# Performance work log

Hardware: AMD Instinct MI355X
Metric: run time of the kernel (lower is better)

The kernel has to match this reference:

```python
import jax, jax.numpy as jnp
import numpy as np

IN_F, OUT_F, LAT, RES, K, B = 512, 512, 512, 64, 3, 8
EPS = 1e-08
C_LIN = 1.0 / np.sqrt(LAT)          # EqualizedWeight scale for linear
C_CONV = 1.0 / np.sqrt(IN_F * K * K)  # EqualizedWeight scale for conv


def setup_inputs() -> dict:
    key = jax.random.key(0)
    k1, k2, k3, k4 = jax.random.split(key, 4)
    return {
        "x": jax.random.normal(k1, (B, IN_F, RES, RES), dtype=jnp.float32),
        "latent": jax.random.normal(k2, (B, LAT), dtype=jnp.float32),
        "w_lin": jax.random.normal(k3, (IN_F, LAT), dtype=jnp.float32),
        "b_lin": jnp.ones((IN_F,), dtype=jnp.float32),
        "w_conv": jax.random.normal(k4, (OUT_F, IN_F, K, K), dtype=jnp.float32),
        "b_conv": jnp.zeros((OUT_F,), dtype=jnp.float32),
    }


def reference(x, latent, w_lin, b_lin, w_conv, b_conv):
    # EqualizedLinear: s = latent @ (w_lin*c).T + b_lin*lr_mul  -> [B, IN_F]
    s = latent @ (w_lin * C_LIN).T + b_lin
    # ModulatedConv2d. Per-sample weight w[b,o,i,k,k] = (w_conv*c)[o,i,k,k]*s[b,i],
    # demodulated by sigma_inv[b,o] = rsqrt(sum_{i,k,k} w^2 + eps).
    w = w_conv * C_CONV  # [O, I, K, K]
    # sum_{k,k} w^2 over spatial -> [O, I], then contract with s^2 -> [B, O]
    w2 = jnp.sum(w * w, axis=(2, 3))  # [O, I]
    sigma_inv = jax.lax.rsqrt(jnp.einsum('oi,bi->bo', w2, s * s) + EPS)
    # conv(x, w*s_b) == conv(x * s_b, w): modulate input, single batched conv,
    # then demodulate output per (b, o). Avoids materializing B*O filters.
    x_mod = x * s[:, :, None, None]
    y = jax.lax.conv_general_dilated(
        x_mod, w,
        window_strides=(1, 1),
        padding=[((K - 1) // 2, (K - 1) // 2)] * 2,
        dimension_numbers=('NCHW', 'OIHW', 'NCHW'),
    )
    y = y * sigma_inv[:, :, None, None] + b_conv[None, :, None, None]
    return y
```

## Files before the change

### kernel.cpp

```cpp
#include <hip/hip_runtime.h>
#include <hip/hip_bf16.h>

#define IN_F 512
#define OUT_F 512
#define LATD 512
#define RES 64
#define BATCH 8
#define EPSV 1e-8f

static constexpr float C_LIN  = 0.04419417382415922f;
static constexpr float C_CONV = 0.014731391274719739f;

typedef __attribute__((ext_vector_type(8)))  short short8;
typedef __attribute__((ext_vector_type(16))) float f32x16;

union BF { __hip_bfloat16 h; short s; };

__device__ __forceinline__ void async_load16(const char* g, char* l) {
  __builtin_amdgcn_global_load_lds(
      (const __attribute__((address_space(1))) unsigned int*)g,
      (__attribute__((address_space(3))) unsigned int*)l, 16, 0, 0);
}

__global__ void k_prep(const float* __restrict__ w_conv,
                       short* __restrict__ wb,
                       float* __restrict__ w2,
                       char* __restrict__ xmp,
                       const float* __restrict__ latent,
                       const float* __restrict__ w_lin,
                       const float* __restrict__ b_lin,
                       float* __restrict__ s) {
  const int t = blockIdx.x * 256 + threadIdx.x;
  {
    const int o = t >> 9;
    const int i = t & 511;
    const float* src = w_conv + (size_t)t * 9;
    const int c = i >> 4, hf0 = (i >> 3) & 1, ch = i & 7;
    const int ob = o >> 7, ol = o & 127;
    short* dst = wb + (size_t)(c * 4 + ob) * 18432 + hf0 * 1024 + ol * 8 + ch;
    float sum = 0.f;
#pragma unroll
    for (int tap = 0; tap < 9; ++tap) {
      const float v = src[tap] * C_CONV;
      sum += v * v;
      BF cv; cv.h = __float2bfloat16(v);
      dst[tap * 2048] = cv.s;
    }
    w2[t] = sum;
  }

  if (blockIdx.x < 256) {
    char* base = xmp + (size_t)blockIdx.x * 139392;
    for (int q = threadIdx.x; q < 520; q += 256) {
      int h, hf, w;
      if (q < 132)      { h = 0;  hf = (q >= 66) ? 1 : 0; w = q - hf * 66; }
      else if (q < 264) { const int r = q - 132; h = 65; hf = (r >= 66) ? 1 : 0; w = r - hf * 66; }
      else              { const int r = q - 264; h = (r >> 2) + 1; hf = (r >> 1) & 1; w = (r & 1) * 65; }
      *(uint4*)(base + ((size_t)(h * 132 + hf * 66 + w)) * 16) = make_uint4(0u, 0u, 0u, 0u);
    }
  }

  if (blockIdx.x < 128) {
    const int wv = threadIdx.x >> 6, lane = threadIdx.x & 63;
    const int i = blockIdx.x * 4 + wv;
    const float4* wl = (const float4*)(w_lin + (size_t)i * LATD);
    const float4 w0 = wl[lane * 2], w1 = wl[lane * 2 + 1];
    float acc[BATCH];
#pragma unroll
    for (int b = 0; b < BATCH; ++b) {
      const float4* lt = (const float4*)(latent + (size_t)b * LATD);
      const float4 l0 = lt[lane * 2], l1 = lt[lane * 2 + 1];
      acc[b] = w0.x * l0.x + w0.y * l0.y + w0.z * l0.z + w0.w * l0.w +
               w1.x * l1.x + w1.y * l1.y + w1.z * l1.z + w1.w * l1.w;
    }
#pragma unroll
    for (int b = 0; b < BATCH; ++b) {
      float v = acc[b];
#pragma unroll
      for (int off = 32; off > 0; off >>= 1) v += __shfl_down(v, off);
      if (lane == 0) s[b * IN_F + i] = v * C_LIN + b_lin[i];
    }
  }
}

__global__ void k_mod_sigma(const float* __restrict__ x,
                            const float* __restrict__ s,
                            char* __restrict__ xmp,
                            const float* __restrict__ w2,
                            float* __restrict__ sigma_inv) {
  if (blockIdx.x < 128) {
    const int o = blockIdx.x * 4 + (threadIdx.x >> 6);
    const int lane = threadIdx.x & 63;
    float acc[BATCH];
#pragma unroll
    for (int b = 0; b < BATCH; ++b) acc[b] = 0.f;
#pragma unroll
    for (int k = 0; k < 8; ++k) {
      const int i = k * 64 + lane;
      const float w = w2[o * IN_F + i];
#pragma unroll
      for (int b = 0; b < BATCH; ++b) {
        const float sv = s[b * IN_F + i];
        acc[b] += w * sv * sv;
      }
    }
#pragma unroll
    for (int b = 0; b < BATCH; ++b) {
      float v = acc[b];
#pragma unroll
      for (int off = 32; off > 0; off >>= 1) v += __shfl_down(v, off);
      if (lane == 0) sigma_inv[b * OUT_F + o] = rsqrtf(v + EPSV);
    }
    return;
  }
  const int bid  = blockIdx.x - 128;
  const int h8   = bid & 7;
  const int ic32 = (bid >> 3) & 15;
  const int b    = bid >> 7;
  __shared__ float tile[32][65];
  const int tid = threadIdx.x;
  const int il = tid >> 3, w8 = (tid & 7) * 8;
  const int i  = ic32 * 32 + il;
  const float sv = s[b * IN_F + i];
  const float* xrow = x + (size_t)(b * IN_F + i) * (RES * RES) + w8;
  const int w = tid >> 2, part = tid & 3;
  const int chalf = part >> 1, hf = part & 1;
  const int c = ic32 * 2 + chalf;
  char* dstb = xmp + (size_t)(c * 8 + b) * 139392 + ((size_t)hf * 66 + (w + 1)) * 16;

  float4 v0 = *(const float4*)(xrow + (size_t)(h8 * 8) * RES);
  float4 v1 = *(const float4*)(xrow + (size_t)(h8 * 8) * RES + 4);
#pragma unroll
  for (int hh = 0; hh < 8; ++hh) {
    const int h = h8 * 8 + hh;
    tile[il][w8 + 0] = v0.x * sv; tile[il][w8 + 1] = v0.y * sv;
    tile[il][w8 + 2] = v0.z * sv; tile[il][w8 + 3] = v0.w * sv;
    tile[il][w8 + 4] = v1.x * sv; tile[il][w8 + 5] = v1.y * sv;
    tile[il][w8 + 6] = v1.z * sv; tile[il][w8 + 7] = v1.w * sv;
    float4 n0, n1;
    if (hh < 7) {
      n0 = *(const float4*)(xrow + (size_t)(h + 1) * RES);
      n1 = *(const float4*)(xrow + (size_t)(h + 1) * RES + 4);
    }
    __syncthreads();
    short8 pk;
#pragma unroll
    for (int j = 0; j < 8; ++j) {
      BF cv; cv.h = __float2bfloat16(tile[chalf * 16 + hf * 8 + j][w]);
      pk[j] = cv.s;
    }
    *(short8*)(dstb + (size_t)(h + 1) * 2112) = pk;
    __syncthreads();
    v0 = n0; v1 = n1;
  }
}

__global__ __launch_bounds__(512, 2)
void k_conv(const char* __restrict__ xmp,
            const short* __restrict__ wbg,
            const float* __restrict__ sigma_inv,
            const float* __restrict__ b_conv,
            float* __restrict__ out) {
  __shared__ __align__(16) char lds[115968];
  const int l = blockIdx.x;
  const int ob = (l >> 3) & 3;
  const int b  = l & 7;
  const int h0 = (l >> 5) * 8;
  const int o0 = ob * 128;
  const int tid = threadIdx.x;
  const int wave = tid >> 6, lane = tid & 63;
  const int l31 = lane & 31, half = lane >> 5;
  const int oh = wave >> 2;
  const int q  = wave & 3;
  const int r0 = (q >> 1) * 4;
  const int c0 = (q & 1) * 32;
  const int st = (wave >> 2) & 1;
  const int dseq[3] = {st, st + 1, st ? 0 : 2};

  f32x16 acc[2][4];
#pragma unroll
  for (int i = 0; i < 2; ++i)
#pragma unroll
    for (int j = 0; j < 4; ++j)
#pragma unroll
      for (int r = 0; r < 16; ++r) acc[i][j][r] = 0.f;

  const char* xsrc0 = xmp + (size_t)b * 139392 + (size_t)h0 * 2112;
  const char* wsrc0 = (const char*)wbg + (size_t)ob * 36864;

#pragma unroll
  for (int k = 0; k < 2; ++k) {
    const int j = tid + k * 512;
    async_load16(xsrc0 + j * 16, lds + j * 16);
  }
  if (tid < 296) { const int j = 1024 + tid; async_load16(xsrc0 + j * 16, lds + j * 16); }
#pragma unroll
  for (int k = 0; k < 4; ++k) {
    const int j = tid + k * 512;
    async_load16(wsrc0 + j * 16, lds + 42240 + j * 16);
  }
  if (tid < 256) { const int j = 2048 + tid; async_load16(wsrc0 + j * 16, lds + 42240 + j * 16); }
  __syncthreads();

  for (int ic = 0; ic < 32; ++ic) {
    const int p = ic & 1;
    if (ic + 1 < 32) {
      const char* xs  = xsrc0 + (size_t)(ic + 1) * (8 * 139392);
      const char* wsr = wsrc0 + (size_t)(ic + 1) * 147456;
      char* xd = lds + (p ^ 1) * 21120;
      char* wd = lds + 42240 + (p ^ 1) * 36864;
#pragma unroll
      for (int k = 0; k < 2; ++k) {
        const int j = tid + k * 512;
        async_load16(xs + j * 16, xd + j * 16);
      }
      if (tid < 296) { const int j = 1024 + tid; async_load16(xs + j * 16, xd + j * 16); }
#pragma unroll
      for (int k = 0; k < 4; ++k) {
        const int j = tid + k * 512;
        async_load16(wsr + j * 16, wd + j * 16);
      }
      if (tid < 256) { const int j = 2048 + tid; async_load16(wsr + j * 16, wd + j * 16); }
    }
    const char* xp = lds + p * 21120;
    const char* wp = lds + 42240 + p * 36864;

    short8 br[2][6];
#pragma unroll
    for (int rr = 0; rr < 6; ++rr)
      br[0][rr] = *(const short8*)(
          xp + (((r0 + rr) * 132) + half * 66 + c0 + dseq[0] + l31) * 16);
    short8 a_cur[2], a_nxt[2];
#pragma unroll
    for (int f = 0; f < 2; ++f)
      a_cur[f] = *(const short8*)(
          wp + dseq[0] * 4096 + half * 2048 + (oh * 64 + f * 32 + l31) * 16);

#pragma unroll
    for (int dwi = 0; dwi < 3; ++dwi) {
      const int cb = dwi & 1, nb = cb ^ 1;
      if (dwi < 2) {
        const int dwn = dseq[dwi + 1];
#pragma unroll
        for (int rr = 0; rr < 6; ++rr)
          br[nb][rr] = *(const short8*)(
              xp + (((r0 + rr) * 132) + half * 66 + c0 + dwn + l31) * 16);
      }
#pragma unroll
      for (int dh = 0; dh < 3; ++dh) {
        if (!(dwi == 2 && dh == 2)) {
          const int dh_n = (dh < 2) ? dh + 1 : 0;
          const int dw_n = (dh < 2) ? dseq[dwi] : dseq[dwi + 1];
#pragma unroll
          for (int f = 0; f < 2; ++f)
            a_nxt[f] = *(const short8*)(
                wp + (dh_n * 3 + dw_n) * 4096 + half * 2048 + (oh * 64 + f * 32 + l31) * 16);
        }
        __builtin_amdgcn_s_setprio(1);
#pragma unroll
        for (int tpr = 0; tpr < 4; ++tpr)
#pragma unroll
          for (int f = 0; f < 2; ++f)
            acc[f][tpr] = __builtin_amdgcn_mfma_f32_32x32x16_bf16(
                a_cur[f], br[cb][tpr + dh], acc[f][tpr], 0, 0, 0);
        __builtin_amdgcn_s_setprio(0);
        a_cur[0] = a_nxt[0]; a_cur[1] = a_nxt[1];
      }
    }
    __syncthreads();
  }

#pragma unroll
  for (int f = 0; f < 2; ++f) {
#pragma unroll
    for (int g = 0; g < 4; ++g) {
#pragma unroll
      for (int r = 0; r < 4; ++r) {
        const int o = o0 + oh * 64 + f * 32 + r + 8 * g + 4 * half;
        const float sig  = sigma_inv[b * OUT_F + o];
        const float bias = b_conv[o];
        const int reg = g * 4 + r;
#pragma unroll
        for (int tpr = 0; tpr < 4; ++tpr) {
          const int h = h0 + r0 + tpr;
          const int w = c0 + l31;
          out[(((size_t)(b * OUT_F + o) * RES + h) * RES) + w] =
              acc[f][tpr][reg] * sig + bias;
        }
      }
    }
  }
}

extern "C" void kernel_launch(void* const* d_in, const int* in_sizes, int n_in,
                              void* d_out, int out_size, void* d_ws, size_t ws_size,
                              hipStream_t stream) {
  const float* x      = (const float*)d_in[0];
  const float* latent = (const float*)d_in[1];
  const float* w_lin  = (const float*)d_in[2];
  const float* b_lin  = (const float*)d_in[3];
  const float* w_conv = (const float*)d_in[4];
  const float* b_conv = (const float*)d_in[5];
  float* out = (float*)d_out;

  char* ws = (char*)d_ws;
  char*  xmp       = ws;
  short* wb        = (short*)(ws + 35684352);
  float* w2        = (float*)(ws + 40402944);
  float* s         = (float*)(ws + 41451520);
  float* sigma_inv = (float*)(ws + 41467904);

  k_prep<<<1024, 256, 0, stream>>>(w_conv, wb, w2, xmp, latent, w_lin, b_lin, s);
  k_mod_sigma<<<128 + 1024, 256, 0, stream>>>(x, s, xmp, w2, sigma_inv);
  k_conv<<<256, 512, 0, stream>>>(xmp, wb, sigma_inv, b_conv, out);
}
```

Baseline: 247.2 us.

## Fuse input modulation and bf16 packing into conv kernel's LDS staging

```diff
diff --git a/kernel.cpp b/kernel.cpp
--- a/kernel.cpp
+++ b/kernel.cpp
@@ -25,7 +25,6 @@
 __global__ void k_prep(const float* __restrict__ w_conv,
                        short* __restrict__ wb,
                        float* __restrict__ w2,
-                       char* __restrict__ xmp,
                        const float* __restrict__ latent,
                        const float* __restrict__ w_lin,
                        const float* __restrict__ b_lin,
@@ -49,17 +48,6 @@
     w2[t] = sum;
   }
 
-  if (blockIdx.x < 256) {
-    char* base = xmp + (size_t)blockIdx.x * 139392;
-    for (int q = threadIdx.x; q < 520; q += 256) {
-      int h, hf, w;
-      if (q < 132)      { h = 0;  hf = (q >= 66) ? 1 : 0; w = q - hf * 66; }
-      else if (q < 264) { const int r = q - 132; h = 65; hf = (r >= 66) ? 1 : 0; w = r - hf * 66; }
-      else              { const int r = q - 264; h = (r >> 2) + 1; hf = (r >> 1) & 1; w = (r & 1) * 65; }
-      *(uint4*)(base + ((size_t)(h * 132 + hf * 66 + w)) * 16) = make_uint4(0u, 0u, 0u, 0u);
-    }
-  }
-
   if (blockIdx.x < 128) {
     const int wv = threadIdx.x >> 6, lane = threadIdx.x & 63;
     const int i = blockIdx.x * 4 + wv;
@@ -83,80 +71,74 @@
   }
 }
 
-__global__ void k_mod_sigma(const float* __restrict__ x,
-                            const float* __restrict__ s,
-                            char* __restrict__ xmp,
-                            const float* __restrict__ w2,
-                            float* __restrict__ sigma_inv) {
-  if (blockIdx.x < 128) {
-    const int o = blockIdx.x * 4 + (threadIdx.x >> 6);
-    const int lane = threadIdx.x & 63;
-    float acc[BATCH];
-#pragma unroll
-    for (int b = 0; b < BATCH; ++b) acc[b] = 0.f;
-#pragma unroll
-    for (int k = 0; k < 8; ++k) {
-      const int i = k * 64 + lane;
-      const float w = w2[o * IN_F + i];
-#pragma unroll
-      for (int b = 0; b < BATCH; ++b) {
-        const float sv = s[b * IN_F + i];
-        acc[b] += w * sv * sv;
-      }
-    }
+__global__ void k_sigma(const float* __restrict__ w2,
+                        const float* __restrict__ s,
+                        float* __restrict__ sigma_inv) {
+  const int o = blockIdx.x * 4 + (threadIdx.x >> 6);
+  const int lane = threadIdx.x & 63;
+  float acc[BATCH];
+#pragma unroll
+  for (int b = 0; b < BATCH; ++b) acc[b] = 0.f;
+#pragma unroll
+  for (int k = 0; k < 8; ++k) {
+    const int i = k * 64 + lane;
+    const float w = w2[o * IN_F + i];
 #pragma unroll
     for (int b = 0; b < BATCH; ++b) {
-      float v = acc[b];
-#pragma unroll
-      for (int off = 32; off > 0; off >>= 1) v += __shfl_down(v, off);
-      if (lane == 0) sigma_inv[b * OUT_F + o] = rsqrtf(v + EPSV);
-    }
-    return;
-  }
-  const int bid  = blockIdx.x - 128;
-  const int h8   = bid & 7;
-  const int ic32 = (bid >> 3) & 15;
-  const int b    = bid >> 7;
-  __shared__ float tile[32][65];
-  const int tid = threadIdx.x;
-  const int il = tid >> 3, w8 = (tid & 7) * 8;
-  const int i  = ic32 * 32 + il;
-  const float sv = s[b * IN_F + i];
-  const float* xrow = x + (size_t)(b * IN_F + i) * (RES * RES) + w8;
-  const int w = tid >> 2, part = tid & 3;
-  const int chalf = part >> 1, hf = part & 1;
-  const int c = ic32 * 2 + chalf;
-  char* dstb = xmp + (size_t)(c * 8 + b) * 139392 + ((size_t)hf * 66 + (w + 1)) * 16;
-
-  float4 v0 = *(const float4*)(xrow + (size_t)(h8 * 8) * RES);
-  float4 v1 = *(const float4*)(xrow + (size_t)(h8 * 8) * RES + 4);
-#pragma unroll
-  for (int hh = 0; hh < 8; ++hh) {
-    const int h = h8 * 8 + hh;
-    tile[il][w8 + 0] = v0.x * sv; tile[il][w8 + 1] = v0.y * sv;
-    tile[il][w8 + 2] = v0.z * sv; tile[il][w8 + 3] = v0.w * sv;
-    tile[il][w8 + 4] = v1.x * sv; tile[il][w8 + 5] = v1.y * sv;
-    tile[il][w8 + 6] = v1.z * sv; tile[il][w8 + 7] = v1.w * sv;
-    float4 n0, n1;
-    if (hh < 7) {
-      n0 = *(const float4*)(xrow + (size_t)(h + 1) * RES);
-      n1 = *(const float4*)(xrow + (size_t)(h + 1) * RES + 4);
-    }
-    __syncthreads();
-    short8 pk;
-#pragma unroll
-    for (int j = 0; j < 8; ++j) {
-      BF cv; cv.h = __float2bfloat16(tile[chalf * 16 + hf * 8 + j][w]);
-      pk[j] = cv.s;
-    }
-    *(short8*)(dstb + (size_t)(h + 1) * 2112) = pk;
-    __syncthreads();
-    v0 = n0; v1 = n1;
+      const float sv = s[b * IN_F + i];
+      acc[b] += w * sv * sv;
+    }
+  }
+#pragma unroll
+  for (int b = 0; b < BATCH; ++b) {
+    float v = acc[b];
+#pragma unroll
+    for (int off = 32; off > 0; off >>= 1) v += __shfl_down(v, off);
+    if (lane == 0) sigma_inv[b * OUT_F + o] = rsqrtf(v + EPSV);
+  }
+}
+
+__device__ __forceinline__ void stage_x_load(
+    const float* __restrict__ xb, const float* __restrict__ s,
+    int b, int icn, int h0, int wave, int lane, int hf_s,
+    float xv[3][8], float ss[8]) {
+#pragma unroll
+  for (int j = 0; j < 8; ++j)
+    ss[j] = s[b * IN_F + icn * 16 + hf_s * 8 + j];
+#pragma unroll
+  for (int k = 0; k < 3; ++k) {
+    const int hr = k * 4 + (wave >> 1);
+    const int h = h0 - 1 + hr;
+    const bool ok = (k < 2 || wave < 4) && (h >= 0) && (h < 64);
+#pragma unroll
+    for (int j = 0; j < 8; ++j)
+      xv[k][j] = ok ? xb[((size_t)(icn * 16 + hf_s * 8 + j)) * (RES * RES)
+                        + h * RES + lane]
+                    : 0.f;
+  }
+}
+
+__device__ __forceinline__ void stage_x_write(
+    char* xd, int wave, int lane, int hf_s,
+    const float xv[3][8], const float ss[8]) {
+#pragma unroll
+  for (int k = 0; k < 3; ++k) {
+    if (k < 2 || wave < 4) {
+      const int hr = k * 4 + (wave >> 1);
+      short8 pk;
+#pragma unroll
+      for (int j = 0; j < 8; ++j) {
+        BF cv; cv.h = __float2bfloat16(xv[k][j] * ss[j]);
+        pk[j] = cv.s;
+      }
+      *(short8*)(xd + ((hr * 132) + hf_s * 66 + (lane + 1)) * 16) = pk;
+    }
   }
 }
 
 __global__ __launch_bounds__(512, 2)
-void k_conv(const char* __restrict__ xmp,
+void k_conv(const float* __restrict__ x,
+            const float* __restrict__ s,
             const short* __restrict__ wbg,
             const float* __restrict__ sigma_inv,
             const float* __restrict__ b_conv,
@@ -176,6 +158,7 @@
   const int c0 = (q & 1) * 32;
   const int st = (wave >> 2) & 1;
   const int dseq[3] = {st, st + 1, st ? 0 : 2};
+  const int hf_s = wave & 1;
 
   f32x16 acc[2][4];
 #pragma unroll
@@ -185,36 +168,36 @@
 #pragma unroll
       for (int r = 0; r < 16; ++r) acc[i][j][r] = 0.f;
 
-  const char* xsrc0 = xmp + (size_t)b * 139392 + (size_t)h0 * 2112;
+  const float* xb = x + (size_t)b * IN_F * (RES * RES);
   const char* wsrc0 = (const char*)wbg + (size_t)ob * 36864;
 
-#pragma unroll
-  for (int k = 0; k < 2; ++k) {
-    const int j = tid + k * 512;
-    async_load16(xsrc0 + j * 16, lds + j * 16);
-  }
-  if (tid < 296) { const int j = 1024 + tid; async_load16(xsrc0 + j * 16, lds + j * 16); }
+  float xv[3][8];
+  float ss[8];
+
+  stage_x_load(xb, s, b, 0, h0, wave, lane, hf_s, xv, ss);
 #pragma unroll
   for (int k = 0; k < 4; ++k) {
     const int j = tid + k * 512;
     async_load16(wsrc0 + j * 16, lds + 42240 + j * 16);
   }
   if (tid < 256) { const int j = 2048 + tid; async_load16(wsrc0 + j * 16, lds + 42240 + j * 16); }
+  stage_x_write(lds, wave, lane, hf_s, xv, ss);
+  if (tid < 80) {
+    const int par = tid & 1, col = ((tid >> 1) & 1) * 65;
+    const int hf2 = (tid >> 2) & 1, hr2 = tid >> 3;
+    short8 z;
+#pragma unroll
+    for (int j = 0; j < 8; ++j) z[j] = 0;
+    *(short8*)(lds + par * 21120 + ((hr2 * 132) + hf2 * 66 + col) * 16) = z;
+  }
   __syncthreads();
 
   for (int ic = 0; ic < 32; ++ic) {
     const int p = ic & 1;
     if (ic + 1 < 32) {
-      const char* xs  = xsrc0 + (size_t)(ic + 1) * (8 * 139392);
+      stage_x_load(xb, s, b, ic + 1, h0, wave, lane, hf_s, xv, ss);
       const char* wsr = wsrc0 + (size_t)(ic + 1) * 147456;
-      char* xd = lds + (p ^ 1) * 21120;
       char* wd = lds + 42240 + (p ^ 1) * 36864;
-#pragma unroll
-      for (int k = 0; k < 2; ++k) {
-        const int j = tid + k * 512;
-        async_load16(xs + j * 16, xd + j * 16);
-      }
-      if (tid < 296) { const int j = 1024 + tid; async_load16(xs + j * 16, xd + j * 16); }
 #pragma unroll
       for (int k = 0; k < 4; ++k) {
         const int j = tid + k * 512;
@@ -267,6 +250,9 @@
         a_cur[0] = a_nxt[0]; a_cur[1] = a_nxt[1];
       }
     }
+
+    if (ic + 1 < 32)
+      stage_x_write(lds + (p ^ 1) * 21120, wave, lane, hf_s, xv, ss);
     __syncthreads();
   }
 
@@ -304,13 +290,12 @@
   float* out = (float*)d_out;
 
   char* ws = (char*)d_ws;
-  char*  xmp       = ws;
-  short* wb        = (short*)(ws + 35684352);
-  float* w2        = (float*)(ws + 40402944);
-  float* s         = (float*)(ws + 41451520);
-  float* sigma_inv = (float*)(ws + 41467904);
-
-  k_prep<<<1024, 256, 0, stream>>>(w_conv, wb, w2, xmp, latent, w_lin, b_lin, s);
-  k_mod_sigma<<<128 + 1024, 256, 0, stream>>>(x, s, xmp, w2, sigma_inv);
-  k_conv<<<256, 512, 0, stream>>>(xmp, wb, sigma_inv, b_conv, out);
-}
+  short* wb        = (short*)ws;
+  float* w2        = (float*)(ws + 4718592);
+  float* s         = (float*)(ws + 5767168);
+  float* sigma_inv = (float*)(ws + 5783552);
+
+  k_prep<<<1024, 256, 0, stream>>>(w_conv, wb, w2, latent, w_lin, b_lin, s);
+  k_sigma<<<128, 256, 0, stream>>>(w2, s, sigma_inv);
+  k_conv<<<256, 512, 0, stream>>>(x, s, wb, sigma_inv, b_conv, out);
+}
```

New measurement: 254.7 us. 3.0% more time.
